# Kernel optimization log

Hardware: AMD Instinct MI355X
Metric: run time of the kernel (lower is better)

## Reference

```python
import jax, jax.numpy as jnp
import numpy as np

BATCH_SIZE = 4096
DIM = 512
TEMPERATURE = 0.5
NUM_CLASSES = 100
EPS = 1e-8  # torch CosineSimilarity eps


def setup_inputs() -> dict:
    key = jax.random.key(0)
    k1, k2, k3 = jax.random.split(key, 3)
    z = jax.random.normal(k1, (BATCH_SIZE, DIM), dtype=jnp.float32)
    z_adv = jax.random.normal(k2, (BATCH_SIZE, DIM), dtype=jnp.float32)
    labels = jax.random.randint(k3, (BATCH_SIZE,), 0, NUM_CLASSES, dtype=jnp.int64)
    return {"z": z, "z_adv": z_adv, "labels": labels}


def _normalize(x):
    # torch.nn.CosineSimilarity clamps norm at eps
    n = jnp.sqrt(jnp.sum(x * x, axis=-1, keepdims=True))
    return x / jnp.maximum(n, EPS)


def reference(z, z_adv, labels):
    N = z.shape[0]
    zn = _normalize(z)            # [N, D]
    zan = _normalize(z_adv)       # [N, D]
    # per-sample clean-vs-adv cosine similarity
    sim_adv = jnp.sum(zn * zan, axis=1) / TEMPERATURE      # [N]
    sim_adv_e = jnp.exp(sim_adv)
    # pairwise cosine similarity via normalize + matmul (same math as
    # the broadcasted CosineSimilarity(dim=2) in the original)
    sim = jnp.einsum('nd,md->nm', zn, zn) / TEMPERATURE     # [N, N]
    # mask: same label, off-diagonal
    same = labels[None, :] == labels[:, None]
    mask = same & ~jnp.eye(N, dtype=bool)
    intra = jnp.sum(jnp.exp(sim) * mask.astype(sim.dtype), axis=1)  # [N]
    loss = -jnp.log(sim_adv_e / (sim_adv_e + intra))
    return jnp.sum(loss) / N
```

## Files before the change

kernel.cpp:

```cpp
#include <hip/hip_runtime.h>
#include <math.h>

#define N      4096
#define DIM    512
#define NCLS   100
#define INV_T  2.0f
#define EPSN   1e-8f
#define CAP    96
#define NTMAX  (CAP / 16)
#define FRAG_SHORTS (NTMAX * 16 * 64 * 8)

#define OFF_INTRA (FRAG_SHORTS * 2)
#define OFF_SADV  (OFF_INTRA + CAP * 4)
#define OFF_SLOT  (OFF_SADV  + CAP * 4)
#define OFF_WRED  (OFF_SLOT  + CAP * 4)
#define OFF_CNT   (OFF_WRED  + 4 * 4)
#define SMEM_BYTES (OFF_CNT + 4)

typedef __attribute__((ext_vector_type(8))) short short8;
typedef __attribute__((ext_vector_type(4))) float float4v;

__device__ __forceinline__ float dot8(const float4& a0, const float4& a1,
                                      const float4& b0, const float4& b1) {
    float p = a0.x * b0.x;
    p = fmaf(a0.y, b0.y, p); p = fmaf(a0.z, b0.z, p); p = fmaf(a0.w, b0.w, p);
    p = fmaf(a1.x, b1.x, p); p = fmaf(a1.y, b1.y, p);
    p = fmaf(a1.z, b1.z, p); p = fmaf(a1.w, b1.w, p);
    return p;
}

__device__ __forceinline__ short f2bf(float x) {
    unsigned u = __float_as_uint(x);
    unsigned r = (u + 0x7FFFu + ((u >> 16) & 1u)) >> 16;
    return (short)r;
}

__global__ __launch_bounds__(256, 1)
void ial_fused_kernel(const float* __restrict__ z,
                      const float* __restrict__ za,
                      const int*   __restrict__ labels,
                      float* __restrict__ out) {
    extern __shared__ char smem[];
    short* frag  = (short*)smem;
    float* intra = (float*)(smem + OFF_INTRA);
    float* sadv  = (float*)(smem + OFF_SADV);
    int*   slot  = (int*)  (smem + OFF_SLOT);
    float* wred  = (float*)(smem + OFF_WRED);
    int*   cnt   = (int*)  (smem + OFF_CNT);

    const int c    = blockIdx.x;
    const int tid  = threadIdx.x;
    const int wave = tid >> 6, lane = tid & 63;

    if (tid == 0) *cnt = 0;
    __syncthreads();
    for (int t = tid; t < N; t += 256) {
        if (labels[t] == c) {
            int p = atomicAdd(cnt, 1);
            if (p < CAP) slot[p] = t;
        }
    }
    __syncthreads();
    int m = *cnt; if (m > CAP) m = CAP;
    const int nt = (m + 15) >> 4;

    const int kt_w = lane >> 2, q_w = lane & 3;
    for (int s = wave; s < nt * 16; s += 4) {
        const int tile = s >> 4, col = s & 15;
        short8 v;
        if (s < m) {
            const int j = slot[s];
            const float4* zr = (const float4*)(z  + (size_t)j * DIM);
            const float4* ar = (const float4*)(za + (size_t)j * DIM);
            float4 f0 = zr[lane * 2], f1 = zr[lane * 2 + 1];
            float4 g0 = ar[lane * 2], g1 = ar[lane * 2 + 1];
            float zz  = dot8(f0, f1, f0, f1);
            float aa  = dot8(g0, g1, g0, g1);
            float zad = dot8(f0, f1, g0, g1);
            #pragma unroll
            for (int off = 32; off >= 1; off >>= 1) {
                zz  += __shfl_xor(zz,  off);
                aa  += __shfl_xor(aa,  off);
                zad += __shfl_xor(zad, off);
            }
            const float nz = fmaxf(sqrtf(zz), EPSN);
            const float na = fmaxf(sqrtf(aa), EPSN);
            const float rn = 1.0f / nz;
            if (lane == 0) sadv[s] = zad / (nz * na) * INV_T;
            v[0] = f2bf(f0.x * rn); v[1] = f2bf(f0.y * rn);
            v[2] = f2bf(f0.z * rn); v[3] = f2bf(f0.w * rn);
            v[4] = f2bf(f1.x * rn); v[5] = f2bf(f1.y * rn);
            v[6] = f2bf(f1.z * rn); v[7] = f2bf(f1.w * rn);
        } else {
            v = (short8)0;
        }
        *(short8*)(frag + (((size_t)(tile * 16 + kt_w) * 64 + q_w * 16 + col) * 8)) = v;
    }
    __syncthreads();

    const int q = lane >> 4, col = lane & 15;
    for (int ti = wave; ti < nt; ti += 4) {
        short8 a[16];
        #pragma unroll
        for (int kt = 0; kt < 16; ++kt)
            a[kt] = *(const short8*)(frag + (((ti * 16 + kt) * 64 + lane) * 8));
        float racc0 = 0.f, racc1 = 0.f, racc2 = 0.f, racc3 = 0.f;
        const int irow = ti * 16 + q * 4;
        for (int tj = 0; tj < nt; ++tj) {
            float4v acc = {0.f, 0.f, 0.f, 0.f};
            #pragma unroll
            for (int kt = 0; kt < 16; ++kt) {
                short8 b = *(const short8*)(frag + (((tj * 16 + kt) * 64 + lane) * 8));
                acc = __builtin_amdgcn_mfma_f32_16x16x32_bf16(a[kt], b, acc, 0, 0, 0);
            }
            const int jslot = tj * 16 + col;
            const bool jok = (jslot < m);
            racc0 += (jok && (irow + 0) != jslot) ? __expf(acc[0] * INV_T) : 0.f;
            racc1 += (jok && (irow + 1) != jslot) ? __expf(acc[1] * INV_T) : 0.f;
            racc2 += (jok && (irow + 2) != jslot) ? __expf(acc[2] * INV_T) : 0.f;
            racc3 += (jok && (irow + 3) != jslot) ? __expf(acc[3] * INV_T) : 0.f;
        }
        #pragma unroll
        for (int off = 1; off < 16; off <<= 1) {
            racc0 += __shfl_xor(racc0, off);
            racc1 += __shfl_xor(racc1, off);
            racc2 += __shfl_xor(racc2, off);
            racc3 += __shfl_xor(racc3, off);
        }
        if (col == 0) {
            intra[irow + 0] = racc0;
            intra[irow + 1] = racc1;
            intra[irow + 2] = racc2;
            intra[irow + 3] = racc3;
        }
    }
    __syncthreads();

    float lsum = 0.f;
    for (int s = tid; s < m; s += 256) {
        const float sa = sadv[s];
        lsum += logf(__expf(sa) + intra[s]) - sa;
    }
    #pragma unroll
    for (int off = 32; off >= 1; off >>= 1) lsum += __shfl_xor(lsum, off);
    if (lane == 0) wred[wave] = lsum;
    __syncthreads();
    if (tid == 0)
        atomicAdd(out, (wred[0] + wred[1] + wred[2] + wred[3]) * (1.0f / (float)N));
}

extern "C" void kernel_launch(void* const* d_in, const int* in_sizes, int n_in,
                              void* d_out, int out_size, void* d_ws, size_t ws_size,
                              hipStream_t stream) {
    const float* z      = (const float*)d_in[0];
    const float* z_adv  = (const float*)d_in[1];
    const int*   labels = (const int*)d_in[2];

    static int attr_done = 0;
    if (!attr_done) {
        hipFuncSetAttribute((const void*)ial_fused_kernel,
                            hipFuncAttributeMaxDynamicSharedMemorySize, SMEM_BYTES);
        attr_done = 1;
    }

    hipMemsetAsync(d_out, 0, sizeof(float), stream);
    ial_fused_kernel<<<NCLS, 256, SMEM_BYTES, stream>>>(z, z_adv, labels,
                                                        (float*)d_out);
}
```

Before: 85.66 us.

## Use 1024-thread blocks, vectorized label scan, and defer norm scaling past MFMA

Blocks grow from 256 to 1024 threads (16 waves), so each class's row loads and MFMA tiles are spread across more waves. The label scan now reads one int4 per thread in a single pass instead of striding. Rows are converted to bf16 unnormalized, and the reciprocal norms are applied to the dot products before the exponential, which takes the normalization multiply off the load path. The risks are a different bf16 rounding from quantizing before normalizing, and extra block-wide sync cost for waves that sit idle when a class has few tiles.

```diff
diff --git a/kernel.cpp b/kernel.cpp
--- a/kernel.cpp
+++ b/kernel.cpp
@@ -9,12 +9,15 @@
 #define CAP    96
 #define NTMAX  (CAP / 16)
 #define FRAG_SHORTS (NTMAX * 16 * 64 * 8)
+#define NTHR   1024
+#define NWAVE  16
 
 #define OFF_INTRA (FRAG_SHORTS * 2)
 #define OFF_SADV  (OFF_INTRA + CAP * 4)
-#define OFF_SLOT  (OFF_SADV  + CAP * 4)
+#define OFF_RNRM  (OFF_SADV  + CAP * 4)
+#define OFF_SLOT  (OFF_RNRM  + CAP * 4)
 #define OFF_WRED  (OFF_SLOT  + CAP * 4)
-#define OFF_CNT   (OFF_WRED  + 4 * 4)
+#define OFF_CNT   (OFF_WRED  + NWAVE * 4)
 #define SMEM_BYTES (OFF_CNT + 4)
 
 typedef __attribute__((ext_vector_type(8))) short short8;
@@ -35,7 +38,7 @@
     return (short)r;
 }
 
-__global__ __launch_bounds__(256, 1)
+__global__ __launch_bounds__(NTHR, 4)
 void ial_fused_kernel(const float* __restrict__ z,
                       const float* __restrict__ za,
                       const int*   __restrict__ labels,
@@ -44,6 +47,7 @@
     short* frag  = (short*)smem;
     float* intra = (float*)(smem + OFF_INTRA);
     float* sadv  = (float*)(smem + OFF_SADV);
+    float* rnrm  = (float*)(smem + OFF_RNRM);
     int*   slot  = (int*)  (smem + OFF_SLOT);
     float* wred  = (float*)(smem + OFF_WRED);
     int*   cnt   = (int*)  (smem + OFF_CNT);
@@ -54,18 +58,20 @@
 
     if (tid == 0) *cnt = 0;
     __syncthreads();
-    for (int t = tid; t < N; t += 256) {
-        if (labels[t] == c) {
-            int p = atomicAdd(cnt, 1);
-            if (p < CAP) slot[p] = t;
-        }
+    {
+        int4 l4 = ((const int4*)labels)[tid];
+        const int b = tid * 4;
+        if (l4.x == c) { int p = atomicAdd(cnt, 1); if (p < CAP) slot[p] = b; }
+        if (l4.y == c) { int p = atomicAdd(cnt, 1); if (p < CAP) slot[p] = b + 1; }
+        if (l4.z == c) { int p = atomicAdd(cnt, 1); if (p < CAP) slot[p] = b + 2; }
+        if (l4.w == c) { int p = atomicAdd(cnt, 1); if (p < CAP) slot[p] = b + 3; }
     }
     __syncthreads();
     int m = *cnt; if (m > CAP) m = CAP;
     const int nt = (m + 15) >> 4;
 
     const int kt_w = lane >> 2, q_w = lane & 3;
-    for (int s = wave; s < nt * 16; s += 4) {
+    for (int s = wave; s < nt * 16; s += NWAVE) {
         const int tile = s >> 4, col = s & 15;
         short8 v;
         if (s < m) {
@@ -74,6 +80,8 @@
             const float4* ar = (const float4*)(za + (size_t)j * DIM);
             float4 f0 = zr[lane * 2], f1 = zr[lane * 2 + 1];
             float4 g0 = ar[lane * 2], g1 = ar[lane * 2 + 1];
+            v[0] = f2bf(f0.x); v[1] = f2bf(f0.y); v[2] = f2bf(f0.z); v[3] = f2bf(f0.w);
+            v[4] = f2bf(f1.x); v[5] = f2bf(f1.y); v[6] = f2bf(f1.z); v[7] = f2bf(f1.w);
             float zz  = dot8(f0, f1, f0, f1);
             float aa  = dot8(g0, g1, g0, g1);
             float zad = dot8(f0, f1, g0, g1);
@@ -83,29 +91,32 @@
                 aa  += __shfl_xor(aa,  off);
                 zad += __shfl_xor(zad, off);
             }
-            const float nz = fmaxf(sqrtf(zz), EPSN);
-            const float na = fmaxf(sqrtf(aa), EPSN);
-            const float rn = 1.0f / nz;
-            if (lane == 0) sadv[s] = zad / (nz * na) * INV_T;
-            v[0] = f2bf(f0.x * rn); v[1] = f2bf(f0.y * rn);
-            v[2] = f2bf(f0.z * rn); v[3] = f2bf(f0.w * rn);
-            v[4] = f2bf(f1.x * rn); v[5] = f2bf(f1.y * rn);
-            v[6] = f2bf(f1.z * rn); v[7] = f2bf(f1.w * rn);
+            if (lane == 0) {
+                const float nz = fmaxf(sqrtf(zz), EPSN);
+                const float na = fmaxf(sqrtf(aa), EPSN);
+                rnrm[s] = 1.0f / nz;
+                sadv[s] = zad / (nz * na) * INV_T;
+            }
         } else {
             v = (short8)0;
+            if (lane == 0) { rnrm[s] = 0.f; sadv[s] = 0.f; }
         }
         *(short8*)(frag + (((size_t)(tile * 16 + kt_w) * 64 + q_w * 16 + col) * 8)) = v;
     }
     __syncthreads();
 
     const int q = lane >> 4, col = lane & 15;
-    for (int ti = wave; ti < nt; ti += 4) {
+    for (int ti = wave; ti < nt; ti += NWAVE) {
         short8 a[16];
         #pragma unroll
         for (int kt = 0; kt < 16; ++kt)
             a[kt] = *(const short8*)(frag + (((ti * 16 + kt) * 64 + lane) * 8));
+        const int irow = ti * 16 + q * 4;
+        const float rni0 = rnrm[irow + 0] * INV_T;
+        const float rni1 = rnrm[irow + 1] * INV_T;
+        const float rni2 = rnrm[irow + 2] * INV_T;
+        const float rni3 = rnrm[irow + 3] * INV_T;
         float racc0 = 0.f, racc1 = 0.f, racc2 = 0.f, racc3 = 0.f;
-        const int irow = ti * 16 + q * 4;
         for (int tj = 0; tj < nt; ++tj) {
             float4v acc = {0.f, 0.f, 0.f, 0.f};
             #pragma unroll
@@ -115,10 +126,11 @@
             }
             const int jslot = tj * 16 + col;
             const bool jok = (jslot < m);
-            racc0 += (jok && (irow + 0) != jslot) ? __expf(acc[0] * INV_T) : 0.f;
-            racc1 += (jok && (irow + 1) != jslot) ? __expf(acc[1] * INV_T) : 0.f;
-            racc2 += (jok && (irow + 2) != jslot) ? __expf(acc[2] * INV_T) : 0.f;
-            racc3 += (jok && (irow + 3) != jslot) ? __expf(acc[3] * INV_T) : 0.f;
+            const float rnj = rnrm[jslot];
+            racc0 += (jok && (irow + 0) != jslot) ? __expf(acc[0] * rni0 * rnj) : 0.f;
+            racc1 += (jok && (irow + 1) != jslot) ? __expf(acc[1] * rni1 * rnj) : 0.f;
+            racc2 += (jok && (irow + 2) != jslot) ? __expf(acc[2] * rni2 * rnj) : 0.f;
+            racc3 += (jok && (irow + 3) != jslot) ? __expf(acc[3] * rni3 * rnj) : 0.f;
         }
         #pragma unroll
         for (int off = 1; off < 16; off <<= 1) {
@@ -137,7 +149,7 @@
     __syncthreads();
 
     float lsum = 0.f;
-    for (int s = tid; s < m; s += 256) {
+    for (int s = tid; s < m; s += NTHR) {
         const float sa = sadv[s];
         lsum += logf(__expf(sa) + intra[s]) - sa;
     }
@@ -145,8 +157,12 @@
     for (int off = 32; off >= 1; off >>= 1) lsum += __shfl_xor(lsum, off);
     if (lane == 0) wred[wave] = lsum;
     __syncthreads();
-    if (tid == 0)
-        atomicAdd(out, (wred[0] + wred[1] + wred[2] + wred[3]) * (1.0f / (float)N));
+    if (tid == 0) {
+        float t = 0.f;
+        #pragma unroll
+        for (int w = 0; w < NWAVE; ++w) t += wred[w];
+        atomicAdd(out, t * (1.0f / (float)N));
+    }
 }
 
 extern "C" void kernel_launch(void* const* d_in, const int* in_sizes, int n_in,
@@ -164,6 +180,6 @@
     }
 
     hipMemsetAsync(d_out, 0, sizeof(float), stream);
-    ial_fused_kernel<<<NCLS, 256, SMEM_BYTES, stream>>>(z, z_adv, labels,
-                                                        (float*)d_out);
+    ial_fused_kernel<<<NCLS, NTHR, SMEM_BYTES, stream>>>(z, z_adv, labels,
+                                                         (float*)d_out);
 }
```

After: 75.69 us. 1.13x faster.
